# Optimization experiments

Hardware: AMD Instinct MI355X
Metric: run time of the kernel (lower is better)

Reference implementation:

```python
import jax, jax.numpy as jnp
import numpy as np

N_NODES = 20000
N_EDGES = 320000
HIDDEN = 64
M = 8            # extra per-node sample axis implied by Linear2's (N, B, M) layout
IN_DIM = 1
OUT_DIM = 1
N_LAYERS = 5
BN_EPS = 1e-5


def setup_inputs() -> dict:
    key = jax.random.key(0)
    ks = jax.random.split(key, 10)
    x = jax.random.normal(ks[0], (N_NODES, IN_DIM, M), dtype=jnp.float32)
    edge_index = jax.random.randint(ks[1], (2, N_EDGES), 0, N_NODES, dtype=jnp.int64)
    batch = jnp.zeros((N_NODES,), dtype=jnp.int64)
    s = 0.1
    w1_0 = jax.random.normal(ks[2], (HIDDEN, IN_DIM), dtype=jnp.float32) * s
    w1 = jax.random.normal(ks[3], (N_LAYERS - 1, HIDDEN, HIDDEN), dtype=jnp.float32) * s
    b1 = jax.random.normal(ks[4], (N_LAYERS, HIDDEN), dtype=jnp.float32) * s
    w2 = jax.random.normal(ks[5], (N_LAYERS, HIDDEN, HIDDEN), dtype=jnp.float32) * s
    b2 = jax.random.normal(ks[6], (N_LAYERS, HIDDEN), dtype=jnp.float32) * s
    gamma = jnp.ones((N_LAYERS, HIDDEN), dtype=jnp.float32)
    beta = jnp.zeros((N_LAYERS, HIDDEN), dtype=jnp.float32)
    w_out = jax.random.normal(ks[7], (OUT_DIM, HIDDEN), dtype=jnp.float32) * s
    b_out = jnp.zeros((OUT_DIM,), dtype=jnp.float32)
    return {"x": x, "edge_index": edge_index, "batch": batch,
            "w1_0": w1_0, "w1": w1, "b1": b1, "w2": w2, "b2": b2,
            "gamma": gamma, "beta": beta, "w_out": w_out, "b_out": b_out}


def reference(x, edge_index, batch, w1_0, w1, b1, w2, b2, gamma, beta, w_out, b_out):
    src, dst = edge_index[0], edge_index[1]
    n = x.shape[0]
    h = x  # [N, C, M]
    for i in range(N_LAYERS):
        # GINConv (eps=0): nn(x + sum of neighbor features scattered by dst)
        agg = jax.ops.segment_sum(h[src], dst, num_segments=n)
        z = h + agg
        W1 = w1_0 if i == 0 else w1[i - 1]
        # Linear2 applies the linear over the channel axis (axis 1)
        z = jnp.einsum('ncm,oc->nom', z, W1) + b1[i][None, :, None]
        z = jax.nn.relu(z)
        z = jnp.einsum('ncm,oc->nom', z, w2[i]) + b2[i][None, :, None]
        z = jax.nn.relu(z)
        # BatchNorm1d over (N, C, M): per-channel stats over N and M (training-mode batch stats)
        mean = z.mean(axis=(0, 2), keepdims=True)
        var = z.var(axis=(0, 2), keepdims=True)
        z = (z - mean) * jax.lax.rsqrt(var + BN_EPS)
        z = z * gamma[i][None, :, None] + beta[i][None, :, None]
        # Dropout(0.5) treated as identity (eval behavior, deterministic reference)
        h = z
    # global mean pool with batch of all zeros -> single graph
    pooled = h.mean(axis=0, keepdims=True)          # [1, H, M]
    pooled = jnp.transpose(pooled, (0, 2, 1))        # [1, M, H]
    out = jax.nn.sigmoid(jnp.einsum('bmh,oh->bmo', pooled, w_out) + b_out)
    return out  # [1, M, OUT_DIM]
```

## Files before the change

### kernel.cpp

```cpp
#include <hip/hip_runtime.h>

#define N_NODES 20000
#define N_EDGES 320000
#define HID 64
#define MDIM 8
#define ROW 512
#define NM 160000.0f
#define NCHUNK 79
#define NSHADOW 16
#define POOLSH 16
#define ZSTRIDE 72
#define ZERO_NODE N_NODES
#define ESRC_CAP 400000

typedef unsigned int uint;
typedef unsigned char uchar;
typedef unsigned short ushort;
typedef __attribute__((ext_vector_type(8))) short bf16x8;
typedef __attribute__((ext_vector_type(4))) float f32x4;
typedef __attribute__((ext_vector_type(2))) float f32x2;

union U4B8 { uint4 u; bf16x8 b; };

__device__ __forceinline__ float bflo(uint u) { return __uint_as_float(u << 16); }
__device__ __forceinline__ float bfhi(uint u) { return __uint_as_float(u & 0xffff0000u); }
__device__ __forceinline__ uint f2bf(float f) {
    uint u = __float_as_uint(f);
    return (u + 0x7fffu + ((u >> 16) & 1u)) >> 16;
}
__device__ __forceinline__ uint pack2(float lo, float hi) { return f2bf(lo) | (f2bf(hi) << 16); }
__device__ __forceinline__ uint2 pkfp8(uint4 pk) {
    int lo = 0, hi = 0;
    lo = __builtin_amdgcn_cvt_pk_fp8_f32(bflo(pk.x), bfhi(pk.x), lo, false);
    lo = __builtin_amdgcn_cvt_pk_fp8_f32(bflo(pk.y), bfhi(pk.y), lo, true);
    hi = __builtin_amdgcn_cvt_pk_fp8_f32(bflo(pk.z), bfhi(pk.z), hi, false);
    hi = __builtin_amdgcn_cvt_pk_fp8_f32(bflo(pk.w), bfhi(pk.w), hi, true);
    uint2 r; r.x = (uint)lo; r.y = (uint)hi; return r;
}

__global__ __launch_bounds__(256) void k_hist(const int* __restrict__ dst, int* __restrict__ deg) {
    int e = blockIdx.x * 256 + threadIdx.x;
    if (e < N_EDGES) atomicAdd(&deg[dst[e]], 1);
}

__global__ __launch_bounds__(256) void k_csum(const int* __restrict__ deg, int* __restrict__ csum) {
    __shared__ int r[256];
    int t = threadIdx.x, i = blockIdx.x * 256 + t;
    r[t] = (i < N_NODES) ? ((deg[i] + 3) & ~3) : 0;
    __syncthreads();
    for (int s = 128; s > 0; s >>= 1) { if (t < s) r[t] += r[t + s]; __syncthreads(); }
    if (t == 0) csum[blockIdx.x] = r[0];
}

__global__ __launch_bounds__(128) void k_cscan(const int* __restrict__ csum, int* __restrict__ chunkoff) {
    __shared__ int s[128];
    int t = threadIdx.x;
    s[t] = (t < NCHUNK) ? csum[t] : 0;
    __syncthreads();
    if (t == 0) { int run = 0; for (int j = 0; j < NCHUNK; ++j) { int x = s[j]; s[j] = run; run += x; } }
    __syncthreads();
    if (t < NCHUNK) chunkoff[t] = s[t];
}

__global__ __launch_bounds__(256) void k_chunkscan(const int* __restrict__ deg, const int* __restrict__ chunkoff,
                                                   int* __restrict__ offs) {
    __shared__ int sd[256];
    int t = threadIdx.x, i = blockIdx.x * 256 + t;
    int v = (i < N_NODES) ? ((deg[i] + 3) & ~3) : 0;
    sd[t] = v;
    __syncthreads();
    for (int off = 1; off < 256; off <<= 1) {
        int x = (t >= off) ? sd[t - off] : 0;
        __syncthreads();
        sd[t] += x;
        __syncthreads();
    }
    if (i < N_NODES) offs[i] = sd[t] - v + chunkoff[blockIdx.x];
}

__global__ __launch_bounds__(256) void k_fill(const int* __restrict__ src, const int* __restrict__ dst,
                                              const int* __restrict__ offs, int* __restrict__ cursor,
                                              int* __restrict__ esrc) {
    int e = blockIdx.x * 256 + threadIdx.x;
    if (e < N_EDGES) {
        int d = dst[e];
        int p = atomicAdd(&cursor[d], 1);
        esrc[offs[d] + p] = src[e];
    }
}

__global__ __launch_bounds__(256) void k_pad(const int* __restrict__ deg, const int* __restrict__ offs,
                                             int* __restrict__ esrc) {
    int id = blockIdx.x * 256 + threadIdx.x;
    if (id >= N_NODES * 4) return;
    int n = id >> 2, s = id & 3;
    int dg = deg[n], pdg = (dg + 3) & ~3;
    int p = dg + s;
    if (p < pdg) esrc[offs[n] + p] = ZERO_NODE;
}

__global__ __launch_bounds__(256) void k_prep(const float* __restrict__ w1, const float* __restrict__ w2,
                                              uint4* __restrict__ wfrag) {
    int id = blockIdx.x * 256 + threadIdx.x;
    if (id >= 4608) return;
    const float* W;
    int s;
    if (id < 4096) {
        int layer = id >> 10;
        int rem = id & 1023;
        int which = rem >> 9;
        s = rem & 511;
        W = which ? &w2[(size_t)(layer + 1) * 4096] : &w1[(size_t)layer * 4096];
    } else {
        s = id - 4096;
        W = w2;
    }
    int f = s >> 6, l = s & 63;
    int o = (f >> 1) * 16 + (l & 15);
    int c0 = (f & 1) * 32 + (l >> 4) * 8;
    const float* p = &W[o * 64 + c0];
    uint4 a;
    a.x = pack2(p[0], p[1]); a.y = pack2(p[2], p[3]);
    a.z = pack2(p[4], p[5]); a.w = pack2(p[6], p[7]);
    wfrag[id] = a;
}

__global__ __launch_bounds__(256) void k_layer0(const float* __restrict__ x, const int* __restrict__ offs,
                                                const int* __restrict__ deg, const int* __restrict__ esrc,
                                                const float* __restrict__ W10, const float* __restrict__ B1,
                                                const uint4* __restrict__ w2f0, const float* __restrict__ B2,
                                                uchar* __restrict__ zout8, float* __restrict__ shadow) {
    __shared__ uint4 w2s[512];
    __shared__ __align__(16) ushort zbuf[128 * ZSTRIDE];
    int tid = threadIdx.x;
    for (int s2 = tid; s2 < 512; s2 += 256) w2s[s2] = w2f0[s2];
    __syncthreads();
    int w = tid >> 6, t = tid & 63;
    int n0 = blockIdx.x * 16 + w * 4;
    int g = t >> 3, m = t & 7;
    float zin0v[4];
    #pragma unroll
    for (int i = 0; i < 4; ++i) {
        int n = n0 + i;
        int off = offs[n], dg = deg[n];
        float acc = (t < 8) ? x[n * 8 + t] : 0.f;
        for (int base = 0; base < dg; base += 8) {
            int k = base + g;
            float v = 0.f;
            if (k < dg) { int nb = esrc[off + k]; v = x[(size_t)nb * 8 + m]; }
            acc += v;
        }
        acc += __shfl_xor(acc, 8);
        acc += __shfl_xor(acc, 16);
        acc += __shfl_xor(acc, 32);
        zin0v[i] = acc;
    }
    bf16x8 bfr[2][2];
    #pragma unroll
    for (int q2 = 0; q2 < 2; ++q2) {
        int kb = q2 * 32 + (t >> 4) * 8;
        float4 wA = *(const float4*)&W10[kb];
        float4 wB = *(const float4*)&W10[kb + 4];
        float4 bA = *(const float4*)&B1[kb];
        float4 bB = *(const float4*)&B1[kb + 4];
        #pragma unroll
        for (int tau = 0; tau < 2; ++tau) {
            float zv = zin0v[tau * 2 + ((t & 15) >> 3)];
            U4B8 u;
            u.u.x = pack2(fmaxf(fmaf(wA.x, zv, bA.x), 0.f), fmaxf(fmaf(wA.y, zv, bA.y), 0.f));
            u.u.y = pack2(fmaxf(fmaf(wA.z, zv, bA.z), 0.f), fmaxf(fmaf(wA.w, zv, bA.w), 0.f));
            u.u.z = pack2(fmaxf(fmaf(wB.x, zv, bB.x), 0.f), fmaxf(fmaf(wB.y, zv, bB.y), 0.f));
            u.u.w = pack2(fmaxf(fmaf(wB.z, zv, bB.z), 0.f), fmaxf(fmaf(wB.w, zv, bB.w), 0.f));
            bfr[q2][tau] = u.b;
        }
    }
    f32x4 acc[4][2];
    #pragma unroll
    for (int o4 = 0; o4 < 4; ++o4) {
        float4 bv = *(const float4*)&B2[o4 * 16 + (t >> 4) * 4];
        #pragma unroll
        for (int tau = 0; tau < 2; ++tau) acc[o4][tau] = (f32x4){bv.x, bv.y, bv.z, bv.w};
    }
    #pragma unroll
    for (int o4 = 0; o4 < 4; ++o4)
        #pragma unroll
        for (int q2 = 0; q2 < 2; ++q2) {
            U4B8 a; a.u = w2s[(o4 * 2 + q2) * 64 + t];
            #pragma unroll
            for (int tau = 0; tau < 2; ++tau)
                acc[o4][tau] = __builtin_amdgcn_mfma_f32_16x16x32_bf16(a.b, bfr[q2][tau], acc[o4][tau], 0, 0, 0);
        }
    #pragma unroll
    for (int o4 = 0; o4 < 4; ++o4)
        #pragma unroll
        for (int tau = 0; tau < 2; ++tau) {
            acc[o4][tau][0] = fmaxf(acc[o4][tau][0], 0.f);
            acc[o4][tau][1] = fmaxf(acc[o4][tau][1], 0.f);
            acc[o4][tau][2] = fmaxf(acc[o4][tau][2], 0.f);
            acc[o4][tau][3] = fmaxf(acc[o4][tau][3], 0.f);
        }
    int sid = (blockIdx.x & (NSHADOW - 1)) * 128;
    #pragma unroll
    for (int o4 = 0; o4 < 4; ++o4)
        #pragma unroll
        for (int r = 0; r < 4; ++r) {
            float x0 = acc[o4][0][r], x1 = acc[o4][1][r];
            float sv = x0 + x1;
            float ssv = x0 * x0 + x1 * x1;
            sv += __shfl_xor(sv, 1);  ssv += __shfl_xor(ssv, 1);
            sv += __shfl_xor(sv, 2);  ssv += __shfl_xor(ssv, 2);
            sv += __shfl_xor(sv, 4);  ssv += __shfl_xor(ssv, 4);
            sv += __shfl_xor(sv, 8);  ssv += __shfl_xor(ssv, 8);
            if ((t & 15) == o4 * 4 + r) {
                int ch = o4 * 16 + (t >> 4) * 4 + r;
                atomicAdd(&shadow[sid + ch], sv);
                atomicAdd(&shadow[sid + 64 + ch], ssv);
            }
        }
    #pragma unroll
    for (int o4 = 0; o4 < 4; ++o4)
        #pragma unroll
        for (int tau = 0; tau < 2; ++tau) {
            uint* p = (uint*)&zbuf[(w * 32 + tau * 16 + (t & 15)) * ZSTRIDE + o4 * 16 + (t >> 4) * 4];
            p[0] = pack2(acc[o4][tau][0], acc[o4][tau][1]);
            p[1] = pack2(acc[o4][tau][2], acc[o4][tau][3]);
        }
    #pragma unroll
    for (int i = 0; i < 4; ++i) {
        uint4 pk = *(const uint4*)&zbuf[(w * 32 + i * 8 + (t >> 3)) * ZSTRIDE + (t & 7) * 8];
        ((uint2*)(zout8 + (size_t)(n0 + i) * ROW))[t] = pkfp8(pk);
    }
}

#define PAIRLD(rr, jj) do { \
    int nb_l = __builtin_amdgcn_readlane(idx, (jj)); \
    int nb_h = __builtin_amdgcn_readlane(idx, (jj) + 1); \
    int nb_ = hi ? nb_h : nb_l; \
    rr = ((const uint4*)(zprev8 + (size_t)nb_ * ROW))[q]; \
} while (0)

#define ACC16(rr) do { \
    f32x2 p_; \
    p_ = __builtin_amdgcn_cvt_pk_f32_fp8((int)rr.x, false); s0  += p_.x; s1  += p_.y; \
    p_ = __builtin_amdgcn_cvt_pk_f32_fp8((int)rr.x, true);  s2  += p_.x; s3  += p_.y; \
    p_ = __builtin_amdgcn_cvt_pk_f32_fp8((int)rr.y, false); s4  += p_.x; s5  += p_.y; \
    p_ = __builtin_amdgcn_cvt_pk_f32_fp8((int)rr.y, true);  s6  += p_.x; s7  += p_.y; \
    p_ = __builtin_amdgcn_cvt_pk_f32_fp8((int)rr.z, false); s8  += p_.x; s9  += p_.y; \
    p_ = __builtin_amdgcn_cvt_pk_f32_fp8((int)rr.z, true);  s10 += p_.x; s11 += p_.y; \
    p_ = __builtin_amdgcn_cvt_pk_f32_fp8((int)rr.w, false); s12 += p_.x; s13 += p_.y; \
    p_ = __builtin_amdgcn_cvt_pk_f32_fp8((int)rr.w, true);  s14 += p_.x; s15 += p_.y; \
} while (0)

__global__ __launch_bounds__(64) __attribute__((amdgpu_waves_per_eu(2, 4)))
void k_layer(const uchar* __restrict__ zprev8,
             const float* __restrict__ shadow_prev,
             const float* __restrict__ gammaP, const float* __restrict__ betaP,
             const int* __restrict__ offs, const int* __restrict__ deg,
             const int* __restrict__ esrc,
             const uint4* __restrict__ w1f, const float* __restrict__ B1,
             const uint4* __restrict__ w2f, const float* __restrict__ B2,
             uchar* __restrict__ zout8, float* __restrict__ shadow) {
    __shared__ __align__(16) ushort zbuf[32 * ZSTRIDE];
    __shared__ __align__(16) float abl[128];
    int t = threadIdx.x;
    int n0 = blockIdx.x * 4;
    int q = t & 31;
    int hi = t >> 5;
    int offv[4], dgv[4], pdgv[4], idxv[4];
    uint2 selfv[4];
    #pragma unroll
    for (int i = 0; i < 4; ++i) {
        offv[i] = offs[n0 + i];
        dgv[i] = deg[n0 + i];
        pdgv[i] = (dgv[i] + 3) & ~3;
    }
    #pragma unroll
    for (int i = 0; i < 4; ++i) idxv[i] = (t < pdgv[i]) ? esrc[offv[i] + t] : 0;
    #pragma unroll
    for (int i = 0; i < 4; ++i) selfv[i] = ((const uint2*)(zprev8 + (size_t)(n0 + i) * ROW))[q * 2 + hi];
    {
        float s = 0.f, ss = 0.f;
        #pragma unroll
        for (int j = 0; j < NSHADOW; ++j) {
            s  += shadow_prev[j * 128 + t];
            ss += shadow_prev[j * 128 + 64 + t];
        }
        float mean = s * (1.f / NM);
        float var = ss * (1.f / NM) - mean * mean;
        float a = gammaP[t] * rsqrtf(var + 1e-5f);
        abl[t] = a;
        abl[64 + t] = betaP[t] - mean * a;
    }
    __syncthreads();
    const float4* abp = (const float4*)abl;
    #pragma unroll
    for (int i = 0; i < 4; ++i) {
        int off = offv[i], dg = dgv[i], pdg = pdgv[i];
        float s0 = 0.f, s1 = 0.f, s2 = 0.f, s3 = 0.f, s4 = 0.f, s5 = 0.f, s6 = 0.f, s7 = 0.f;
        float s8 = 0.f, s9 = 0.f, s10 = 0.f, s11 = 0.f, s12 = 0.f, s13 = 0.f, s14 = 0.f, s15 = 0.f;
        for (int base = 0; base < pdg; base += 64) {
            int cnt = pdg - base; if (cnt > 64) cnt = 64;
            int idx = base ? ((t < cnt) ? esrc[off + base + t] : 0) : idxv[i];
            int j = 0;
            for (; j + 16 <= cnt; j += 16) {
                uint4 r0, r1, r2, r3, r4, r5, r6, r7;
                PAIRLD(r0, j);      PAIRLD(r1, j + 2);  PAIRLD(r2, j + 4);  PAIRLD(r3, j + 6);
                PAIRLD(r4, j + 8);  PAIRLD(r5, j + 10); PAIRLD(r6, j + 12); PAIRLD(r7, j + 14);
                ACC16(r0); ACC16(r1); ACC16(r2); ACC16(r3);
                ACC16(r4); ACC16(r5); ACC16(r6); ACC16(r7);
            }
            if (cnt - j >= 8) {
                uint4 r0, r1, r2, r3;
                PAIRLD(r0, j); PAIRLD(r1, j + 2); PAIRLD(r2, j + 4); PAIRLD(r3, j + 6);
                ACC16(r0); ACC16(r1); ACC16(r2); ACC16(r3);
                j += 8;
            }
            if (cnt - j >= 4) {
                uint4 r0, r1;
                PAIRLD(r0, j); PAIRLD(r1, j + 2);
                ACC16(r0); ACC16(r1);
            }
        }
        float u, r0, r1, r2, r3, r4, r5, r6, r7;
        u = hi ? s0 : s8;   r0 = (hi ? s8  : s0) + __shfl_xor(u, 32);
        u = hi ? s1 : s9;   r1 = (hi ? s9  : s1) + __shfl_xor(u, 32);
        u = hi ? s2 : s10;  r2 = (hi ? s10 : s2) + __shfl_xor(u, 32);
        u = hi ? s3 : s11;  r3 = (hi ? s11 : s3) + __shfl_xor(u, 32);
        u = hi ? s4 : s12;  r4 = (hi ? s12 : s4) + __shfl_xor(u, 32);
        u = hi ? s5 : s13;  r5 = (hi ? s13 : s5) + __shfl_xor(u, 32);
        u = hi ? s6 : s14;  r6 = (hi ? s14 : s6) + __shfl_xor(u, 32);
        u = hi ? s7 : s15;  r7 = (hi ? s15 : s7) + __shfl_xor(u, 32);
        {
            uint2 sv = selfv[i];
            f32x2 p_;
            p_ = __builtin_amdgcn_cvt_pk_f32_fp8((int)sv.x, false); r0 += p_.x; r1 += p_.y;
            p_ = __builtin_amdgcn_cvt_pk_f32_fp8((int)sv.x, true);  r2 += p_.x; r3 += p_.y;
            p_ = __builtin_amdgcn_cvt_pk_f32_fp8((int)sv.y, false); r4 += p_.x; r5 += p_.y;
            p_ = __builtin_amdgcn_cvt_pk_f32_fp8((int)sv.y, true);  r6 += p_.x; r7 += p_.y;
        }
        int c4 = (q & 3) * 4 + hi * 2;
        float4 Af0 = abp[c4], Af1 = abp[c4 + 1];
        float4 Bf0 = abp[16 + c4], Bf1 = abp[16 + c4 + 1];
        float dp1 = (float)(dg + 1);
        uint4 pk;
        pk.x = pack2(fmaf(Af0.x, r0, Bf0.x * dp1), fmaf(Af0.y, r1, Bf0.y * dp1));
        pk.y = pack2(fmaf(Af0.z, r2, Bf0.z * dp1), fmaf(Af0.w, r3, Bf0.w * dp1));
        pk.z = pack2(fmaf(Af1.x, r4, Bf1.x * dp1), fmaf(Af1.y, r5, Bf1.y * dp1));
        pk.w = pack2(fmaf(Af1.z, r6, Bf1.z * dp1), fmaf(Af1.w, r7, Bf1.w * dp1));
        *(uint4*)&zbuf[(i * 8 + (q >> 2)) * ZSTRIDE + (q & 3) * 16 + hi * 8] = pk;
    }
    bf16x8 bfr[2][2];
    #pragma unroll
    for (int tau = 0; tau < 2; ++tau)
        #pragma unroll
        for (int q2 = 0; q2 < 2; ++q2) {
            U4B8 u;
            u.u = *(const uint4*)&zbuf[(tau * 16 + (t & 15)) * ZSTRIDE + q2 * 32 + (t >> 4) * 8];
            bfr[q2][tau] = u.b;
        }
    f32x4 acc[4][2];
    #pragma unroll
    for (int o4 = 0; o4 < 4; ++o4) {
        float4 bv = *(const float4*)&B1[o4 * 16 + (t >> 4) * 4];
        #pragma unroll
        for (int tau = 0; tau < 2; ++tau) acc[o4][tau] = (f32x4){bv.x, bv.y, bv.z, bv.w};
    }
    #pragma unroll
    for (int o4 = 0; o4 < 4; ++o4)
        #pragma unroll
        for (int q2 = 0; q2 < 2; ++q2) {
            U4B8 a; a.u = w1f[(o4 * 2 + q2) * 64 + t];
            #pragma unroll
            for (int tau = 0; tau < 2; ++tau)
                acc[o4][tau] = __builtin_amdgcn_mfma_f32_16x16x32_bf16(a.b, bfr[q2][tau], acc[o4][tau], 0, 0, 0);
        }
    #pragma unroll
    for (int o4 = 0; o4 < 4; ++o4)
        #pragma unroll
        for (int tau = 0; tau < 2; ++tau) {
            f32x4 v = acc[o4][tau];
            float h0 = fmaxf(v[0], 0.f), h1 = fmaxf(v[1], 0.f), h2 = fmaxf(v[2], 0.f), h3 = fmaxf(v[3], 0.f);
            uint* p = (uint*)&zbuf[(tau * 16 + (t & 15)) * ZSTRIDE + o4 * 16 + (t >> 4) * 4];
            p[0] = pack2(h0, h1); p[1] = pack2(h2, h3);
        }
    #pragma unroll
    for (int tau = 0; tau < 2; ++tau)
        #pragma unroll
        for (int q2 = 0; q2 < 2; ++q2) {
            U4B8 u;
            u.u = *(const uint4*)&zbuf[(tau * 16 + (t & 15)) * ZSTRIDE + q2 * 32 + (t >> 4) * 8];
            bfr[q2][tau] = u.b;
        }
    #pragma unroll
    for (int o4 = 0; o4 < 4; ++o4) {
        float4 bv = *(const float4*)&B2[o4 * 16 + (t >> 4) * 4];
        #pragma unroll
        for (int tau = 0; tau < 2; ++tau) acc[o4][tau] = (f32x4){bv.x, bv.y, bv.z, bv.w};
    }
    #pragma unroll
    for (int o4 = 0; o4 < 4; ++o4)
        #pragma unroll
        for (int q2 = 0; q2 < 2; ++q2) {
            U4B8 a; a.u = w2f[(o4 * 2 + q2) * 64 + t];
            #pragma unroll
            for (int tau = 0; tau < 2; ++tau)
                acc[o4][tau] = __builtin_amdgcn_mfma_f32_16x16x32_bf16(a.b, bfr[q2][tau], acc[o4][tau], 0, 0, 0);
        }
    #pragma unroll
    for (int o4 = 0; o4 < 4; ++o4)
        #pragma unroll
        for (int tau = 0; tau < 2; ++tau) {
            acc[o4][tau][0] = fmaxf(acc[o4][tau][0], 0.f);
            acc[o4][tau][1] = fmaxf(acc[o4][tau][1], 0.f);
            acc[o4][tau][2] = fmaxf(acc[o4][tau][2], 0.f);
            acc[o4][tau][3] = fmaxf(acc[o4][tau][3], 0.f);
        }
    int sid = (blockIdx.x & (NSHADOW - 1)) * 128;
    #pragma unroll
    for (int o4 = 0; o4 < 4; ++o4)
        #pragma unroll
        for (int r = 0; r < 4; ++r) {
            float x0 = acc[o4][0][r], x1 = acc[o4][1][r];
            float sv = x0 + x1;
            float ssv = x0 * x0 + x1 * x1;
            sv += __shfl_xor(sv, 1);  ssv += __shfl_xor(ssv, 1);
            sv += __shfl_xor(sv, 2);  ssv += __shfl_xor(ssv, 2);
            sv += __shfl_xor(sv, 4);  ssv += __shfl_xor(ssv, 4);
            sv += __shfl_xor(sv, 8);  ssv += __shfl_xor(ssv, 8);
            if ((t & 15) == o4 * 4 + r) {
                int ch = o4 * 16 + (t >> 4) * 4 + r;
                atomicAdd(&shadow[sid + ch], sv);
                atomicAdd(&shadow[sid + 64 + ch], ssv);
            }
        }
    #pragma unroll
    for (int o4 = 0; o4 < 4; ++o4)
        #pragma unroll
        for (int tau = 0; tau < 2; ++tau) {
            uint* p = (uint*)&zbuf[(tau * 16 + (t & 15)) * ZSTRIDE + o4 * 16 + (t >> 4) * 4];
            p[0] = pack2(acc[o4][tau][0], acc[o4][tau][1]);
            p[1] = pack2(acc[o4][tau][2], acc[o4][tau][3]);
        }
    #pragma unroll
    for (int i = 0; i < 4; ++i) {
        uint4 pk = *(const uint4*)&zbuf[(i * 8 + (t >> 3)) * ZSTRIDE + (t & 7) * 8];
        ((uint2*)(zout8 + (size_t)(n0 + i) * ROW))[t] = pkfp8(pk);
    }
}

__global__ __launch_bounds__(256) void k_pool(const uint* __restrict__ z8, float* __restrict__ pool) {
    int t = blockIdx.x * 256 + threadIdx.x;
    float s0 = 0.f, s1 = 0.f, s2 = 0.f, s3 = 0.f;
    for (int u = t; u < N_NODES * ROW / 4; u += 65536) {
        uint v = z8[u];
        f32x2 p0 = __builtin_amdgcn_cvt_pk_f32_fp8((int)v, false);
        f32x2 p1 = __builtin_amdgcn_cvt_pk_f32_fp8((int)v, true);
        s0 += p0.x; s1 += p0.y; s2 += p1.x; s3 += p1.y;
    }
    int k4 = t & 127;
    int sid = (blockIdx.x & (POOLSH - 1)) * 512;
    atomicAdd(&pool[sid + k4 * 4 + 0], s0);
    atomicAdd(&pool[sid + k4 * 4 + 1], s1);
    atomicAdd(&pool[sid + k4 * 4 + 2], s2);
    atomicAdd(&pool[sid + k4 * 4 + 3], s3);
}

__global__ __launch_bounds__(64) void k_out(const float* __restrict__ pool, const float* __restrict__ shadow4,
                                            const float* __restrict__ gamma4, const float* __restrict__ beta4,
                                            const float* __restrict__ wout, const float* __restrict__ bout,
                                            float* __restrict__ out) {
    int c = threadIdx.x;
    float s = 0.f, ss = 0.f;
    #pragma unroll
    for (int j = 0; j < NSHADOW; ++j) { s += shadow4[j * 128 + c]; ss += shadow4[j * 128 + 64 + c]; }
    float mean = s * (1.f / NM);
    float var = ss * (1.f / NM) - mean * mean;
    float a = gamma4[c] * rsqrtf(var + 1e-5f);
    float b = beta4[c] - mean * a;
    float wv = wout[c];
    for (int m = 0; m < 8; ++m) {
        float pv = 0.f;
        #pragma unroll
        for (int j = 0; j < POOLSH; ++j) pv += pool[j * 512 + m * 64 + c];
        float v = wv * (a * pv * (1.f / N_NODES) + b);
        for (int off = 32; off > 0; off >>= 1) v += __shfl_down(v, off);
        if (c == 0) out[m] = 1.f / (1.f + expf(-(v + bout[0])));
    }
}

extern "C" void kernel_launch(void* const* d_in, const int* in_sizes, int n_in,
                              void* d_out, int out_size, void* d_ws, size_t ws_size,
                              hipStream_t stream) {
    const float* x     = (const float*)d_in[0];
    const int*   ei    = (const int*)d_in[1];
    const int*   srcp  = ei;
    const int*   dstp  = ei + N_EDGES;
    const float* w1_0  = (const float*)d_in[3];
    const float* w1    = (const float*)d_in[4];
    const float* b1    = (const float*)d_in[5];
    const float* w2    = (const float*)d_in[6];
    const float* b2    = (const float*)d_in[7];
    const float* gamma = (const float*)d_in[8];
    const float* beta  = (const float*)d_in[9];
    const float* wout  = (const float*)d_in[10];
    const float* bout  = (const float*)d_in[11];
    float* out = (float*)d_out;

    char* ws = (char*)d_ws;
    size_t off = 0;
    auto alloc = [&](size_t bytes) -> void* {
        void* p = ws + off;
        off = (off + bytes + 255) & ~(size_t)255;
        return p;
    };
    uchar* zA8   = (uchar*)alloc((size_t)(N_NODES + 1) * ROW);
    uchar* zB8   = (uchar*)alloc((size_t)(N_NODES + 1) * ROW);
    uint4* wfrag = (uint4*)alloc(4608 * 16);
    int* deg      = (int*)alloc(N_NODES * 4);
    int* cursor   = (int*)alloc(N_NODES * 4);
    float* shadow = (float*)alloc(5 * NSHADOW * 128 * 4);
    float* pool   = (float*)alloc(POOLSH * 512 * 4);
    size_t zero_bytes = (size_t)((char*)pool - (char*)deg) + POOLSH * 512 * 4;
    int* offs     = (int*)alloc(N_NODES * 4);
    int* esrc     = (int*)alloc(ESRC_CAP * 4);
    int* csum     = (int*)alloc(NCHUNK * 4);
    int* chunkoff = (int*)alloc(NCHUNK * 4);

    hipMemsetAsync(deg, 0, zero_bytes, stream);
    hipMemsetAsync(zA8 + (size_t)N_NODES * ROW, 0, ROW, stream);
    hipMemsetAsync(zB8 + (size_t)N_NODES * ROW, 0, ROW, stream);

    k_hist<<<(N_EDGES + 255) / 256, 256, 0, stream>>>(dstp, deg);
    k_csum<<<NCHUNK, 256, 0, stream>>>(deg, csum);
    k_cscan<<<1, 128, 0, stream>>>(csum, chunkoff);
    k_chunkscan<<<NCHUNK, 256, 0, stream>>>(deg, chunkoff, offs);
    k_fill<<<(N_EDGES + 255) / 256, 256, 0, stream>>>(srcp, dstp, offs, cursor, esrc);
    k_pad<<<(N_NODES * 4 + 255) / 256, 256, 0, stream>>>(deg, offs, esrc);
    k_prep<<<18, 256, 0, stream>>>(w1, w2, wfrag);

    k_layer0<<<N_NODES / 16, 256, 0, stream>>>(x, offs, deg, esrc, w1_0, b1, wfrag + 4096, b2,
                                               zA8, shadow);

    const uchar* zin8 = zA8;
    uchar* zo8 = zB8;
    for (int i = 1; i <= 4; ++i) {
        k_layer<<<N_NODES / 4, 64, 0, stream>>>(zin8,
                                                shadow + (size_t)(i - 1) * NSHADOW * 128,
                                                gamma + (i - 1) * 64, beta + (i - 1) * 64,
                                                offs, deg, esrc,
                                                wfrag + (size_t)(i - 1) * 1024, b1 + i * 64,
                                                wfrag + (size_t)(i - 1) * 1024 + 512, b2 + i * 64,
                                                zo8,
                                                shadow + (size_t)i * NSHADOW * 128);
        const uchar* t8 = zin8; zin8 = zo8; zo8 = (uchar*)t8;
    }

    k_pool<<<256, 256, 0, stream>>>((const uint*)zA8, pool);
    k_out<<<1, 64, 0, stream>>>(pool, shadow + 4 * NSHADOW * 128, gamma + 256, beta + 256, wout, bout, out);
}
```

Baseline: 402.1 us.

## Fuse preprocessing kernels, pad with self-index, and prefetch neighbor indices in layer0

Merges the degree histogram with weight-fragment packing, and edge fill with padding, so fewer kernels are launched. Padding slots now hold the node's own index instead of a dedicated zero row, and the self term is scaled by (1 + deg - padded_deg) to cancel the extra contributions. This removes the zero row and its two memsets. Layer 0 loads up to 64 neighbor indices per node in one coalesced read and broadcasts them with shuffles, which cuts dependent global loads. The price is extra correction arithmetic, and fp8 rounding of the duplicated self value may not cancel exactly.

```diff
diff --git a/kernel.cpp b/kernel.cpp
--- a/kernel.cpp
+++ b/kernel.cpp
@@ -10,7 +10,6 @@
 #define NSHADOW 16
 #define POOLSH 16
 #define ZSTRIDE 72
-#define ZERO_NODE N_NODES
 #define ESRC_CAP 400000
 
 typedef unsigned int uint;
@@ -38,9 +37,33 @@
     uint2 r; r.x = (uint)lo; r.y = (uint)hi; return r;
 }
 
-__global__ __launch_bounds__(256) void k_hist(const int* __restrict__ dst, int* __restrict__ deg) {
-    int e = blockIdx.x * 256 + threadIdx.x;
-    if (e < N_EDGES) atomicAdd(&deg[dst[e]], 1);
+__global__ __launch_bounds__(256) void k_histprep(const int* __restrict__ dst, int* __restrict__ deg,
+                                                  const float* __restrict__ w1, const float* __restrict__ w2,
+                                                  uint4* __restrict__ wfrag) {
+    int id = blockIdx.x * 256 + threadIdx.x;
+    if (id < N_EDGES) { atomicAdd(&deg[dst[id]], 1); return; }
+    int pid = id - N_EDGES;
+    if (pid >= 4608) return;
+    const float* W;
+    int s;
+    if (pid < 4096) {
+        int layer = pid >> 10;
+        int rem = pid & 1023;
+        int which = rem >> 9;
+        s = rem & 511;
+        W = which ? &w2[(size_t)(layer + 1) * 4096] : &w1[(size_t)layer * 4096];
+    } else {
+        s = pid - 4096;
+        W = w2;
+    }
+    int f = s >> 6, l = s & 63;
+    int o = (f >> 1) * 16 + (l & 15);
+    int c0 = (f & 1) * 32 + (l >> 4) * 8;
+    const float* p = &W[o * 64 + c0];
+    uint4 a;
+    a.x = pack2(p[0], p[1]); a.y = pack2(p[2], p[3]);
+    a.z = pack2(p[4], p[5]); a.w = pack2(p[6], p[7]);
+    wfrag[pid] = a;
 }
 
 __global__ __launch_bounds__(256) void k_csum(const int* __restrict__ deg, int* __restrict__ csum) {
@@ -78,51 +101,22 @@
     if (i < N_NODES) offs[i] = sd[t] - v + chunkoff[blockIdx.x];
 }
 
-__global__ __launch_bounds__(256) void k_fill(const int* __restrict__ src, const int* __restrict__ dst,
-                                              const int* __restrict__ offs, int* __restrict__ cursor,
-                                              int* __restrict__ esrc) {
-    int e = blockIdx.x * 256 + threadIdx.x;
-    if (e < N_EDGES) {
-        int d = dst[e];
+__global__ __launch_bounds__(256) void k_fillpad(const int* __restrict__ src, const int* __restrict__ dst,
+                                                 const int* __restrict__ offs, const int* __restrict__ deg,
+                                                 int* __restrict__ cursor, int* __restrict__ esrc) {
+    int id = blockIdx.x * 256 + threadIdx.x;
+    if (id < N_EDGES) {
+        int d = dst[id];
         int p = atomicAdd(&cursor[d], 1);
-        esrc[offs[d] + p] = src[e];
-    }
-}
-
-__global__ __launch_bounds__(256) void k_pad(const int* __restrict__ deg, const int* __restrict__ offs,
-                                             int* __restrict__ esrc) {
-    int id = blockIdx.x * 256 + threadIdx.x;
-    if (id >= N_NODES * 4) return;
-    int n = id >> 2, s = id & 3;
+        esrc[offs[d] + p] = src[id];
+        return;
+    }
+    int pid = id - N_EDGES;
+    if (pid >= N_NODES * 4) return;
+    int n = pid >> 2, s = pid & 3;
     int dg = deg[n], pdg = (dg + 3) & ~3;
     int p = dg + s;
-    if (p < pdg) esrc[offs[n] + p] = ZERO_NODE;
-}
-
-__global__ __launch_bounds__(256) void k_prep(const float* __restrict__ w1, const float* __restrict__ w2,
-                                              uint4* __restrict__ wfrag) {
-    int id = blockIdx.x * 256 + threadIdx.x;
-    if (id >= 4608) return;
-    const float* W;
-    int s;
-    if (id < 4096) {
-        int layer = id >> 10;
-        int rem = id & 1023;
-        int which = rem >> 9;
-        s = rem & 511;
-        W = which ? &w2[(size_t)(layer + 1) * 4096] : &w1[(size_t)layer * 4096];
-    } else {
-        s = id - 4096;
-        W = w2;
-    }
-    int f = s >> 6, l = s & 63;
-    int o = (f >> 1) * 16 + (l & 15);
-    int c0 = (f & 1) * 32 + (l >> 4) * 8;
-    const float* p = &W[o * 64 + c0];
-    uint4 a;
-    a.x = pack2(p[0], p[1]); a.y = pack2(p[2], p[3]);
-    a.z = pack2(p[4], p[5]); a.w = pack2(p[6], p[7]);
-    wfrag[id] = a;
+    if (p < pdg) esrc[offs[n] + p] = n;
 }
 
 __global__ __launch_bounds__(256) void k_layer0(const float* __restrict__ x, const int* __restrict__ offs,
@@ -138,17 +132,28 @@
     int w = tid >> 6, t = tid & 63;
     int n0 = blockIdx.x * 16 + w * 4;
     int g = t >> 3, m = t & 7;
+    int offv[4], dgv[4], idxv[4];
+    #pragma unroll
+    for (int i = 0; i < 4; ++i) { offv[i] = offs[n0 + i]; dgv[i] = deg[n0 + i]; }
+    #pragma unroll
+    for (int i = 0; i < 4; ++i) idxv[i] = (t < dgv[i]) ? esrc[offv[i] + t] : 0;
     float zin0v[4];
     #pragma unroll
     for (int i = 0; i < 4; ++i) {
         int n = n0 + i;
-        int off = offs[n], dg = deg[n];
+        int dg = dgv[i];
         float acc = (t < 8) ? x[n * 8 + t] : 0.f;
-        for (int base = 0; base < dg; base += 8) {
-            int k = base + g;
+        int dgc = dg < 64 ? dg : 64;
+        for (int base = 0; base < dgc; base += 8) {
+            int slot = base + g;
+            int nb = __shfl(idxv[i], slot & 63);
             float v = 0.f;
-            if (k < dg) { int nb = esrc[off + k]; v = x[(size_t)nb * 8 + m]; }
+            if (slot < dg) v = x[(size_t)nb * 8 + m];
             acc += v;
+        }
+        for (int k = 64 + g; k < dg; k += 8) {
+            int nb = esrc[offv[i] + k];
+            acc += x[(size_t)nb * 8 + m];
         }
         acc += __shfl_xor(acc, 8);
         acc += __shfl_xor(acc, 16);
@@ -332,11 +337,12 @@
         u = hi ? s7 : s15;  r7 = (hi ? s15 : s7) + __shfl_xor(u, 32);
         {
             uint2 sv = selfv[i];
+            float cf = (float)(1 + dg - pdg);
             f32x2 p_;
-            p_ = __builtin_amdgcn_cvt_pk_f32_fp8((int)sv.x, false); r0 += p_.x; r1 += p_.y;
-            p_ = __builtin_amdgcn_cvt_pk_f32_fp8((int)sv.x, true);  r2 += p_.x; r3 += p_.y;
-            p_ = __builtin_amdgcn_cvt_pk_f32_fp8((int)sv.y, false); r4 += p_.x; r5 += p_.y;
-            p_ = __builtin_amdgcn_cvt_pk_f32_fp8((int)sv.y, true);  r6 += p_.x; r7 += p_.y;
+            p_ = __builtin_amdgcn_cvt_pk_f32_fp8((int)sv.x, false); r0 = fmaf(cf, p_.x, r0); r1 = fmaf(cf, p_.y, r1);
+            p_ = __builtin_amdgcn_cvt_pk_f32_fp8((int)sv.x, true);  r2 = fmaf(cf, p_.x, r2); r3 = fmaf(cf, p_.y, r3);
+            p_ = __builtin_amdgcn_cvt_pk_f32_fp8((int)sv.y, false); r4 = fmaf(cf, p_.x, r4); r5 = fmaf(cf, p_.y, r5);
+            p_ = __builtin_amdgcn_cvt_pk_f32_fp8((int)sv.y, true);  r6 = fmaf(cf, p_.x, r6); r7 = fmaf(cf, p_.y, r7);
         }
         int c4 = (q & 3) * 4 + hi * 2;
         float4 Af0 = abp[c4], Af1 = abp[c4 + 1];
@@ -513,8 +519,8 @@
         off = (off + bytes + 255) & ~(size_t)255;
         return p;
     };
-    uchar* zA8   = (uchar*)alloc((size_t)(N_NODES + 1) * ROW);
-    uchar* zB8   = (uchar*)alloc((size_t)(N_NODES + 1) * ROW);
+    uchar* zA8   = (uchar*)alloc((size_t)N_NODES * ROW);
+    uchar* zB8   = (uchar*)alloc((size_t)N_NODES * ROW);
     uint4* wfrag = (uint4*)alloc(4608 * 16);
     int* deg      = (int*)alloc(N_NODES * 4);
     int* cursor   = (int*)alloc(N_NODES * 4);
@@ -527,16 +533,12 @@
     int* chunkoff = (int*)alloc(NCHUNK * 4);
 
     hipMemsetAsync(deg, 0, zero_bytes, stream);
-    hipMemsetAsync(zA8 + (size_t)N_NODES * ROW, 0, ROW, stream);
-    hipMemsetAsync(zB8 + (size_t)N_NODES * ROW, 0, ROW, stream);
-
-    k_hist<<<(N_EDGES + 255) / 256, 256, 0, stream>>>(dstp, deg);
+
+    k_histprep<<<(N_EDGES + 4608 + 255) / 256, 256, 0, stream>>>(dstp, deg, w1, w2, wfrag);
     k_csum<<<NCHUNK, 256, 0, stream>>>(deg, csum);
     k_cscan<<<1, 128, 0, stream>>>(csum, chunkoff);
     k_chunkscan<<<NCHUNK, 256, 0, stream>>>(deg, chunkoff, offs);
-    k_fill<<<(N_EDGES + 255) / 256, 256, 0, stream>>>(srcp, dstp, offs, cursor, esrc);
-    k_pad<<<(N_NODES * 4 + 255) / 256, 256, 0, stream>>>(deg, offs, esrc);
-    k_prep<<<18, 256, 0, stream>>>(w1, w2, wfrag);
+    k_fillpad<<<(N_EDGES + N_NODES * 4 + 255) / 256, 256, 0, stream>>>(srcp, dstp, offs, deg, cursor, esrc);
 
     k_layer0<<<N_NODES / 16, 256, 0, stream>>>(x, offs, deg, esrc, w1_0, b1, wfrag + 4096, b2,
                                                zA8, shadow);
```

Measured after the change: 394.4 us (median of 2 runs). About the same (-1.9%).
